# Kernel optimization log

Measured on AMD Instinct MI355X. Metric: run time of the kernel, lower is better.

## Reference

```python
import math
import jax, jax.numpy as jnp
import numpy as np

D_MODEL = 512
MAX_SEQ = 512
NUM_OUT = 16
H = 1  # num_heads


def _pos_encoding(d_model, seq_len):
    # sinusoidal PE, then flipped along the sequence axis (ReversedPositionalEncoding)
    pos = jnp.arange(seq_len, dtype=jnp.float32)[:, None]
    i = jnp.arange(0, d_model, 2, dtype=jnp.float32)
    ang = pos * jnp.exp(i * (-(math.log(10000.0) / d_model)))  # [S, d/2]
    pe = jnp.stack([jnp.sin(ang), jnp.cos(ang)], axis=-1).reshape(seq_len, d_model)
    return pe[::-1]


def _layernorm(x, w, b, eps=1e-5):
    m = jnp.mean(x, axis=-1, keepdims=True)
    v = jnp.mean(jnp.square(x - m), axis=-1, keepdims=True)
    return (x - m) / jnp.sqrt(v + eps) * w + b


def setup_inputs() -> dict:
    key = jax.random.key(0)
    ks = jax.random.split(key, 8)
    B = 128
    latents = jax.random.normal(ks[0], (B, D_MODEL, MAX_SEQ), dtype=jnp.float32)
    query_mask = jnp.ones((B, NUM_OUT), dtype=jnp.float32)
    query = 0.02 * jax.random.normal(ks[1], (NUM_OUT, D_MODEL), dtype=jnp.float32)
    return {
        "latents": latents,
        "query_mask": query_mask,
        "query": query,
        "ln_lat_w": jnp.ones((D_MODEL,), jnp.float32),
        "ln_lat_b": jnp.zeros((D_MODEL,), jnp.float32),
        "ln_q_w": jnp.ones((D_MODEL,), jnp.float32),
        "ln_q_b": jnp.zeros((D_MODEL,), jnp.float32),
        "Wq": 0.02 * jax.random.normal(ks[2], (D_MODEL, D_MODEL), jnp.float32),
        "bq": jnp.zeros((D_MODEL,), jnp.float32),
        "Wk": 0.02 * jax.random.normal(ks[3], (D_MODEL, D_MODEL), jnp.float32),
        "bk": jnp.zeros((D_MODEL,), jnp.float32),
        "Wv": 0.02 * jax.random.normal(ks[4], (D_MODEL, D_MODEL), jnp.float32),
        "bv": jnp.zeros((D_MODEL,), jnp.float32),
        "Wo": 0.02 * jax.random.normal(ks[5], (1, D_MODEL), jnp.float32),
        "bo": jnp.zeros((1,), jnp.float32),
    }


def reference(latents, query_mask, query, ln_lat_w, ln_lat_b, ln_q_w, ln_q_b,
              Wq, bq, Wk, bk, Wv, bv, Wo, bo):
    B, _, N = latents.shape  # latents: [B, d_model, N]
    scale = math.sqrt(D_MODEL)
    Dh = D_MODEL // H

    # cross-attention mask: query_mask [B,Nq] x all-ones latent mask [B,N]
    mask = jnp.einsum('bq,bk->bqk', query_mask, jnp.ones((B, N), latents.dtype))

    x = jnp.swapaxes(latents, 1, 2) * scale           # [B, N, d]
    x = x + _pos_encoding(D_MODEL, MAX_SEQ)[-N:]      # reversed PE, last N positions
    # dropout is identity in eval mode
    x = _layernorm(x, ln_lat_w, ln_lat_b)

    q = _layernorm(query * scale, ln_q_w, ln_q_b)     # [Nq, d]
    q = jnp.broadcast_to(q[None], (B, NUM_OUT, D_MODEL))

    qh = (q @ Wq.T + bq).reshape(B, NUM_OUT, H, Dh)
    kh = (x @ Wk.T + bk).reshape(B, N, H, Dh)
    vh = (x @ Wv.T + bv).reshape(B, N, H, Dh)

    scores = jnp.einsum('bqhd,bkhd->bhqk', qh, kh) / math.sqrt(Dh)
    scores = jnp.where(mask[:, None] == 0, -1e9, scores)
    attn_weights = jax.nn.softmax(scores, axis=-1)    # [B, H, Nq, N]

    attn = jnp.einsum('bhqk,bkhd->bqhd', attn_weights, vh).reshape(B, NUM_OUT, H * Dh)
    wipe = jnp.all(mask == 0, axis=2, keepdims=True)  # [B, Nq, 1]
    attn = jnp.where(wipe, 0.0, attn)

    logits = attn @ Wo.T + bo                         # [B, Nq, 1]
    return logits, attn_weights
```

## Files before the change

kernel.cpp:

```cpp
#include <hip/hip_runtime.h>
#include <math.h>

#define DM 512
#define NQ 16
#define NG (NQ + 1)
#define NR (NG + 2)

typedef __attribute__((ext_vector_type(2))) float f32x2;

__device__ __forceinline__ float wave_reduce_sum(float v) {
    #pragma unroll
    for (int off = 32; off > 0; off >>= 1) v += __shfl_xor(v, off, 64);
    return v;
}
__device__ __forceinline__ float wave_reduce_max(float v) {
    #pragma unroll
    for (int off = 32; off > 0; off >>= 1) v = fmaxf(v, __shfl_xor(v, off, 64));
    return v;
}

__global__ void k1_setup(const float* __restrict__ Wk, const float* __restrict__ Wv,
                         const float* __restrict__ query,
                         const float* __restrict__ ln_q_w, const float* __restrict__ ln_q_b,
                         const float* __restrict__ Wq, const float* __restrict__ bq,
                         float* __restrict__ PET, float* __restrict__ WkT,
                         float* __restrict__ WvT, float* __restrict__ qh, int N) {
    __shared__ float tile[64][65];
    int bx = blockIdx.x;
    int lane = threadIdx.x & 63;
    int w = threadIdx.x >> 6;

    if (bx < 128) {
        int ntile = bx & 7, jg = bx >> 3;
        int n = ntile * 64 + lane;
        float p = (float)(N - 1 - n);
        const float c = -logf(10000.f) / (float)DM;
        int jbase = jg * 16 + w * 4;
        #pragma unroll
        for (int u = 0; u < 4; ++u) {
            int j = jbase + u;
            float wj = expf((float)(2 * j) * c);
            float ang = p * wj;
            PET[(size_t)(2 * j) * N + n] = sinf(ang);
            PET[(size_t)(2 * j + 1) * N + n] = cosf(ang);
        }
    } else if (bx < 256) {
        int t = bx - 128;
        const float* W = (t >> 6) ? Wv : Wk;
        float* WT = (t >> 6) ? WvT : WkT;
        int tl = t & 63;
        int te = tl >> 3, td = tl & 7;
        #pragma unroll
        for (int i = 0; i < 16; ++i) {
            int el = w * 16 + i;
            tile[el][lane] = W[(size_t)(te * 64 + el) * DM + td * 64 + lane];
        }
        __syncthreads();
        #pragma unroll
        for (int i = 0; i < 16; ++i) {
            int dl = w * 16 + i;
            WT[(size_t)(td * 64 + dl) * DM + te * 64 + lane] = tile[lane][dl];
        }
    } else {
        int idx = (bx - 256) * 4 + w;
        int q = idx >> 9, e = idx & 511;
        const float scale = 22.627416997969522f;
        const float4* qr = (const float4*)(query + (size_t)q * DM);
        float4 a0 = qr[lane * 2], a1 = qr[lane * 2 + 1];
        a0.x *= scale; a0.y *= scale; a0.z *= scale; a0.w *= scale;
        a1.x *= scale; a1.y *= scale; a1.z *= scale; a1.w *= scale;
        float s  = a0.x + a0.y + a0.z + a0.w + a1.x + a1.y + a1.z + a1.w;
        float s2 = a0.x * a0.x + a0.y * a0.y + a0.z * a0.z + a0.w * a0.w
                 + a1.x * a1.x + a1.y * a1.y + a1.z * a1.z + a1.w * a1.w;
        s = wave_reduce_sum(s); s2 = wave_reduce_sum(s2);
        float m = s * (1.f / DM);
        float var = s2 * (1.f / DM) - m * m;
        float rstd = rsqrtf(var + 1e-5f);
        const float4* gw = (const float4*)ln_q_w;
        const float4* gb = (const float4*)ln_q_b;
        const float4* wr = (const float4*)(Wq + (size_t)e * DM);
        float4 w0 = gw[lane * 2], w1 = gw[lane * 2 + 1];
        float4 b0 = gb[lane * 2], b1 = gb[lane * 2 + 1];
        float4 W0 = wr[lane * 2], W1 = wr[lane * 2 + 1];
        float acc = ((a0.x - m) * rstd * w0.x + b0.x) * W0.x
                  + ((a0.y - m) * rstd * w0.y + b0.y) * W0.y
                  + ((a0.z - m) * rstd * w0.z + b0.z) * W0.z
                  + ((a0.w - m) * rstd * w0.w + b0.w) * W0.w
                  + ((a1.x - m) * rstd * w1.x + b1.x) * W1.x
                  + ((a1.y - m) * rstd * w1.y + b1.y) * W1.y
                  + ((a1.z - m) * rstd * w1.z + b1.z) * W1.z
                  + ((a1.w - m) * rstd * w1.w + b1.w) * W1.w;
        acc = wave_reduce_sum(acc);
        if (lane == 0) qh[q * DM + e] = acc + bq[e];
    }
}

__global__ void k3_qt(const float* __restrict__ qh, const float* __restrict__ WkT,
                      const float* __restrict__ Wo, const float* __restrict__ WvT,
                      const float* __restrict__ lnw,
                      float* __restrict__ qt, float* __restrict__ A,
                      f32x2* __restrict__ A2, float* __restrict__ wvout) {
    int idx = blockIdx.x * 4 + (threadIdx.x >> 6);
    int lane = threadIdx.x & 63;
    int g = idx >> 9, d = idx & 511;
    const float4* wr;
    const float4* xr;
    if (g < NQ) {
        wr = (const float4*)(WkT + (size_t)d * DM);
        xr = (const float4*)(qh + (size_t)g * DM);
    } else {
        wr = (const float4*)(WvT + (size_t)d * DM);
        xr = (const float4*)Wo;
    }
    float4 w0 = wr[lane * 2], w1 = wr[lane * 2 + 1];
    float4 x0 = xr[lane * 2], x1 = xr[lane * 2 + 1];
    float s = w0.x * x0.x + w0.y * x0.y + w0.z * x0.z + w0.w * x0.w
            + w1.x * x1.x + w1.y * x1.y + w1.z * x1.z + w1.w * x1.w;
    s = wave_reduce_sum(s);
    if (lane == 0) {
        if (g < NQ) qt[g * DM + d] = s;
        else wvout[d] = s;
        float a = s * lnw[d];
        A[g * DM + d] = a;
        f32x2 ap; ap.x = a; ap.y = a;
        A2[g * DM + d] = ap;
    }
}

__launch_bounds__(256, 4)
__global__ void main2_kernel(const float* __restrict__ latents,
                             const float* __restrict__ PET,
                             const f32x2* __restrict__ A2,
                             const float* __restrict__ A,
                             const float* __restrict__ qt,
                             const float* __restrict__ qh,
                             const float* __restrict__ wv,
                             const float* __restrict__ lnb,
                             const float* __restrict__ bk,
                             const float* __restrict__ Wo,
                             const float* __restrict__ bv,
                             float* __restrict__ pbuf,
                             float* __restrict__ consts, int N) {
    int B = gridDim.y - 1;
    int lane = threadIdx.x & 63;
    int w = threadIdx.x >> 6;
    int b = blockIdx.y;

    if (b == B) {
        int t = blockIdx.x * 4 + w;
        if (t > NQ) return;
        if (t < NQ) {
            float sa = 0.f, sc = 0.f, qb = 0.f;
            #pragma unroll
            for (int i = 0; i < 8; ++i) {
                int d = i * 64 + lane;
                sa += A[t * DM + d];
                sc = fmaf(qt[t * DM + d], lnb[d], sc);
                qb = fmaf(qh[t * DM + d], bk[d], qb);
            }
            sa = wave_reduce_sum(sa);
            sc = wave_reduce_sum(sc);
            qb = wave_reduce_sum(qb);
            if (lane == 0) { consts[t] = sa; consts[16 + t] = sc + qb; }
        } else {
            float sa = 0.f, cv = 0.f, bvo = 0.f;
            #pragma unroll
            for (int i = 0; i < 8; ++i) {
                int d = i * 64 + lane;
                sa += A[NQ * DM + d];
                cv = fmaf(wv[d], lnb[d], cv);
                bvo = fmaf(Wo[d], bv[d], bvo);
            }
            sa = wave_reduce_sum(sa);
            cv = wave_reduce_sum(cv);
            bvo = wave_reduce_sum(bvo);
            if (lane == 0) { consts[32] = sa; consts[33] = cv + bvo; }
        }
        return;
    }

    int ntiles = N >> 7;
    int ntile = blockIdx.x % ntiles;
    int dh = blockIdx.x / ntiles;
    int n0 = ntile * 128 + lane * 2;

    int d0 = __builtin_amdgcn_readfirstlane(dh * 256 + w * 64);
    const float* latf = latents + (size_t)b * DM * N + (size_t)d0 * N + n0;
    const float* petf = PET + (size_t)d0 * N + n0;
    const float scale = 22.627416997969522f;
    f32x2 sc2; sc2.x = scale; sc2.y = scale;

    f32x2 acc[NG];
    #pragma unroll
    for (int i = 0; i < NG; ++i) { acc[i].x = 0.f; acc[i].y = 0.f; }
    f32x2 S1 = {0.f, 0.f}, S2 = {0.f, 0.f};

    const int U = 4;
    const int NC = 64 / U;
    f32x2 xb[2][U], pb[2][U];
    #pragma unroll
    for (int u = 0; u < U; ++u) {
        xb[0][u] = __builtin_nontemporal_load((const f32x2*)(latf + (size_t)u * N));
        pb[0][u] = *(const f32x2*)(petf + (size_t)u * N);
    }
    for (int c = 0; c < NC; c += 2) {
        #pragma unroll
        for (int u = 0; u < U; ++u) {
            size_t dd = (size_t)((c + 1) * U + u) * N;
            xb[1][u] = __builtin_nontemporal_load((const f32x2*)(latf + dd));
            pb[1][u] = *(const f32x2*)(petf + dd);
        }
        #pragma unroll
        for (int u = 0; u < U; ++u) {
            f32x2 y = xb[0][u] * sc2 + pb[0][u];
            S1 += y; S2 += y * y;
            int d = d0 + c * U + u;
            #pragma unroll
            for (int q = 0; q < NG; ++q)
                acc[q] += A2[(size_t)q * DM + d] * y;
        }
        if (c + 2 < NC) {
            #pragma unroll
            for (int u = 0; u < U; ++u) {
                size_t dd = (size_t)((c + 2) * U + u) * N;
                xb[0][u] = __builtin_nontemporal_load((const f32x2*)(latf + dd));
                pb[0][u] = *(const f32x2*)(petf + dd);
            }
        }
        #pragma unroll
        for (int u = 0; u < U; ++u) {
            f32x2 y = xb[1][u] * sc2 + pb[1][u];
            S1 += y; S2 += y * y;
            int d = d0 + (c + 1) * U + u;
            #pragma unroll
            for (int q = 0; q < NG; ++q)
                acc[q] += A2[(size_t)q * DM + d] * y;
        }
    }

    __shared__ f32x2 red[4][NR][64];
    red[w][0][lane] = S1;
    red[w][1][lane] = S2;
    #pragma unroll
    for (int i = 0; i < NG; ++i) red[w][2 + i][lane] = acc[i];
    __syncthreads();
    if (w != 0) return;

    float* pout = pbuf + (((size_t)dh * B + b) * NR) * N + n0;
    #pragma unroll
    for (int i = 0; i < NR; ++i) {
        f32x2 t = red[0][i][lane] + red[1][i][lane] + red[2][i][lane] + red[3][i][lane];
        *(f32x2*)(pout + (size_t)i * N) = t;
    }
}

__global__ void k_fin(const float* __restrict__ pbuf,
                      const float* __restrict__ consts,
                      const float* __restrict__ query_mask,
                      const float* __restrict__ bo,
                      float* __restrict__ out_logits,
                      float* __restrict__ out_attn, int N, int B) {
    __shared__ float scs[NQ][512];
    __shared__ float vls[512];
    int b = blockIdx.x;
    int tid = threadIdx.x;
    const float isd = 0.044194173824159216f;
    float c32 = consts[32], c33 = consts[33];

    for (int np = tid; np < (N >> 1); np += 256) {
        int n0 = np * 2;
        const float* p0 = pbuf + (((size_t)0 * B + b) * NR) * N + n0;
        const float* p1 = pbuf + (((size_t)1 * B + b) * NR) * N + n0;
        f32x2 tot[NR];
        #pragma unroll
        for (int i = 0; i < NR; ++i)
            tot[i] = *(const f32x2*)(p0 + (size_t)i * N)
                   + *(const f32x2*)(p1 + (size_t)i * N);
        f32x2 m = tot[0] * (1.f / DM);
        f32x2 ex2 = tot[1] * (1.f / DM);
        f32x2 rstd;
        rstd.x = rsqrtf(ex2.x - m.x * m.x + 1e-5f);
        rstd.y = rsqrtf(ex2.y - m.y * m.y + 1e-5f);
        f32x2 v = rstd * (tot[2 + NQ] - m * c32) + c33;
        *(f32x2*)&vls[n0] = v;
        #pragma unroll
        for (int q = 0; q < NQ; ++q) {
            f32x2 sc = (rstd * (tot[2 + q] - m * consts[q]) + consts[16 + q]) * isd;
            *(f32x2*)&scs[q][n0] = sc;
        }
    }
    __syncthreads();

    int lane = tid & 63, w = tid >> 6;
    int nv = N >> 2;
    for (int q = w; q < NQ; q += 4) {
        int r = b * NQ + q;
        float qm = query_mask[r];
        float4* arow = (float4*)(out_attn + (size_t)r * N);
        if (qm == 0.f) {
            float u = 1.f / (float)N;
            float4 uv = make_float4(u, u, u, u);
            for (int i = lane; i < nv; i += 64) arow[i] = uv;
            if (lane == 0) out_logits[r] = bo[0];
            continue;
        }
        const float4* srow = (const float4*)scs[q];
        float4 sv[2];
        sv[0] = srow[lane]; sv[1] = srow[64 + lane];
        float mx = fmaxf(fmaxf(fmaxf(sv[0].x, sv[0].y), fmaxf(sv[0].z, sv[0].w)),
                         fmaxf(fmaxf(sv[1].x, sv[1].y), fmaxf(sv[1].z, sv[1].w)));
        mx = wave_reduce_max(mx);
        float sum = 0.f;
        #pragma unroll
        for (int i = 0; i < 2; ++i) {
            sv[i].x = expf(sv[i].x - mx); sv[i].y = expf(sv[i].y - mx);
            sv[i].z = expf(sv[i].z - mx); sv[i].w = expf(sv[i].w - mx);
            sum += sv[i].x + sv[i].y + sv[i].z + sv[i].w;
        }
        sum = wave_reduce_sum(sum);
        float inv = 1.f / sum;
        const float4* vrow = (const float4*)vls;
        float lp = 0.f;
        #pragma unroll
        for (int i = 0; i < 2; ++i) {
            float4 vv = vrow[i * 64 + lane];
            float4 wgt;
            wgt.x = sv[i].x * inv; wgt.y = sv[i].y * inv;
            wgt.z = sv[i].z * inv; wgt.w = sv[i].w * inv;
            arow[i * 64 + lane] = wgt;
            lp += wgt.x * vv.x + wgt.y * vv.y + wgt.z * vv.z + wgt.w * vv.w;
        }
        lp = wave_reduce_sum(lp);
        if (lane == 0) out_logits[r] = lp + bo[0];
    }
}

extern "C" void kernel_launch(void* const* d_in, const int* in_sizes, int n_in,
                              void* d_out, int out_size, void* d_ws, size_t ws_size,
                              hipStream_t stream) {
    const float* latents    = (const float*)d_in[0];
    const float* query_mask = (const float*)d_in[1];
    const float* query      = (const float*)d_in[2];
    const float* ln_lat_w   = (const float*)d_in[3];
    const float* ln_lat_b   = (const float*)d_in[4];
    const float* ln_q_w     = (const float*)d_in[5];
    const float* ln_q_b     = (const float*)d_in[6];
    const float* Wq         = (const float*)d_in[7];
    const float* bq         = (const float*)d_in[8];
    const float* Wk         = (const float*)d_in[9];
    const float* bk         = (const float*)d_in[10];
    const float* Wv         = (const float*)d_in[11];
    const float* bv         = (const float*)d_in[12];
    const float* Wo         = (const float*)d_in[13];
    const float* bo         = (const float*)d_in[14];

    int B = in_sizes[1] / NQ;
    int N = in_sizes[0] / (DM * B);

    float* ws = (float*)d_ws;
    size_t off = 0;
    float* PET    = ws + off; off += (size_t)DM * N;
    float* WkT    = ws + off; off += (size_t)DM * DM;
    float* WvT    = ws + off; off += (size_t)DM * DM;
    float* qh     = ws + off; off += NQ * DM;
    float* qt     = ws + off; off += NQ * DM;
    float* A      = ws + off; off += NG * DM;
    float* A2     = ws + off; off += (size_t)NG * DM * 2;
    float* wv     = ws + off; off += DM;
    float* consts = ws + off; off += 64;
    float* pbuf   = ws + off; off += (size_t)2 * B * NR * N;

    float* out_logits = (float*)d_out;
    float* out_attn   = out_logits + (size_t)B * NQ;

    k1_setup<<<256 + NQ * DM / 4, 256, 0, stream>>>(
        Wk, Wv, query, ln_q_w, ln_q_b, Wq, bq, PET, WkT, WvT, qh, N);
    k3_qt<<<NG * DM / 4, 256, 0, stream>>>(qh, WkT, Wo, WvT, ln_lat_w,
                                           qt, A, (f32x2*)A2, wv);
    dim3 gmain((N >> 7) * 2, B + 1);
    main2_kernel<<<gmain, 256, 0, stream>>>(latents, PET, (const f32x2*)A2,
                                            A, qt, qh, wv, ln_lat_b, bk, Wo, bv,
                                            pbuf, consts, N);
    k_fin<<<B, 256, 0, stream>>>(pbuf, consts, query_mask, bo,
                                 out_logits, out_attn, N, B);
}
```

Baseline: 240.9 us.

## Cover full d_model per block with 8 waves and drop split partial buffer

The main kernel now launches 512-thread blocks. Each block spans all 512 feature rows for a 128-column tile, where before two blocks each covered half the rows. The 8 wave partials are reduced in two LDS stages, so the pbuf partial buffer halves and k_fin no longer sums two halves. The attention-weight stores in k_fin become nontemporal vector stores. The main kernel gets half as many blocks, larger blocks and an extra barrier, which may lower occupancy and grid parallelism.

After: 240.0 us (median of 2 runs). No clear change (-0.4%).

```diff
diff --git a/kernel.cpp b/kernel.cpp
--- a/kernel.cpp
+++ b/kernel.cpp
@@ -7,6 +7,7 @@
 #define NR (NG + 2)
 
 typedef __attribute__((ext_vector_type(2))) float f32x2;
+typedef __attribute__((ext_vector_type(4))) float f32x4;
 
 __device__ __forceinline__ float wave_reduce_sum(float v) {
     #pragma unroll
@@ -127,7 +128,7 @@
     }
 }
 
-__launch_bounds__(256, 4)
+__launch_bounds__(512, 4)
 __global__ void main2_kernel(const float* __restrict__ latents,
                              const float* __restrict__ PET,
                              const f32x2* __restrict__ A2,
@@ -147,7 +148,7 @@
     int b = blockIdx.y;
 
     if (b == B) {
-        int t = blockIdx.x * 4 + w;
+        int t = blockIdx.x * 8 + w;
         if (t > NQ) return;
         if (t < NQ) {
             float sa = 0.f, sc = 0.f, qb = 0.f;
@@ -179,12 +180,10 @@
         return;
     }
 
-    int ntiles = N >> 7;
-    int ntile = blockIdx.x % ntiles;
-    int dh = blockIdx.x / ntiles;
+    int ntile = blockIdx.x;
     int n0 = ntile * 128 + lane * 2;
 
-    int d0 = __builtin_amdgcn_readfirstlane(dh * 256 + w * 64);
+    int d0 = __builtin_amdgcn_readfirstlane(w * 64);
     const float* latf = latents + (size_t)b * DM * N + (size_t)d0 * N + n0;
     const float* petf = PET + (size_t)d0 * N + n0;
     const float scale = 22.627416997969522f;
@@ -239,18 +238,29 @@
     }
 
     __shared__ f32x2 red[4][NR][64];
-    red[w][0][lane] = S1;
-    red[w][1][lane] = S2;
-    #pragma unroll
-    for (int i = 0; i < NG; ++i) red[w][2 + i][lane] = acc[i];
+    if (w >= 4) {
+        int ww = w - 4;
+        red[ww][0][lane] = S1;
+        red[ww][1][lane] = S2;
+        #pragma unroll
+        for (int i = 0; i < NG; ++i) red[ww][2 + i][lane] = acc[i];
+    }
     __syncthreads();
-    if (w != 0) return;
-
-    float* pout = pbuf + (((size_t)dh * B + b) * NR) * N + n0;
-    #pragma unroll
-    for (int i = 0; i < NR; ++i) {
-        f32x2 t = red[0][i][lane] + red[1][i][lane] + red[2][i][lane] + red[3][i][lane];
-        *(f32x2*)(pout + (size_t)i * N) = t;
+    if (w < 4) {
+        red[w][0][lane] += S1;
+        red[w][1][lane] += S2;
+        #pragma unroll
+        for (int i = 0; i < NG; ++i) red[w][2 + i][lane] += acc[i];
+    }
+    __syncthreads();
+    if (w == 0) {
+        float* pout = pbuf + ((size_t)b * NR) * N + n0;
+        #pragma unroll
+        for (int i = 0; i < NR; ++i) {
+            f32x2 t = red[0][i][lane] + red[1][i][lane]
+                    + red[2][i][lane] + red[3][i][lane];
+            *(f32x2*)(pout + (size_t)i * N) = t;
+        }
     }
 }
 
@@ -269,13 +279,10 @@
 
     for (int np = tid; np < (N >> 1); np += 256) {
         int n0 = np * 2;
-        const float* p0 = pbuf + (((size_t)0 * B + b) * NR) * N + n0;
-        const float* p1 = pbuf + (((size_t)1 * B + b) * NR) * N + n0;
+        const float* p = pbuf + ((size_t)b * NR) * N + n0;
         f32x2 tot[NR];
         #pragma unroll
-        for (int i = 0; i < NR; ++i)
-            tot[i] = *(const f32x2*)(p0 + (size_t)i * N)
-                   + *(const f32x2*)(p1 + (size_t)i * N);
+        for (int i = 0; i < NR; ++i) tot[i] = *(const f32x2*)(p + (size_t)i * N);
         f32x2 m = tot[0] * (1.f / DM);
         f32x2 ex2 = tot[1] * (1.f / DM);
         f32x2 rstd;
@@ -296,16 +303,17 @@
     for (int q = w; q < NQ; q += 4) {
         int r = b * NQ + q;
         float qm = query_mask[r];
-        float4* arow = (float4*)(out_attn + (size_t)r * N);
+        f32x4* arow = (f32x4*)(out_attn + (size_t)r * N);
         if (qm == 0.f) {
             float u = 1.f / (float)N;
-            float4 uv = make_float4(u, u, u, u);
-            for (int i = lane; i < nv; i += 64) arow[i] = uv;
+            f32x4 uv; uv.x = u; uv.y = u; uv.z = u; uv.w = u;
+            for (int i = lane; i < nv; i += 64)
+                __builtin_nontemporal_store(uv, &arow[i]);
             if (lane == 0) out_logits[r] = bo[0];
             continue;
         }
-        const float4* srow = (const float4*)scs[q];
-        float4 sv[2];
+        const f32x4* srow = (const f32x4*)scs[q];
+        f32x4 sv[2];
         sv[0] = srow[lane]; sv[1] = srow[64 + lane];
         float mx = fmaxf(fmaxf(fmaxf(sv[0].x, sv[0].y), fmaxf(sv[0].z, sv[0].w)),
                          fmaxf(fmaxf(sv[1].x, sv[1].y), fmaxf(sv[1].z, sv[1].w)));
@@ -319,15 +327,13 @@
         }
         sum = wave_reduce_sum(sum);
         float inv = 1.f / sum;
-        const float4* vrow = (const float4*)vls;
+        const f32x4* vrow = (const f32x4*)vls;
         float lp = 0.f;
         #pragma unroll
         for (int i = 0; i < 2; ++i) {
-            float4 vv = vrow[i * 64 + lane];
-            float4 wgt;
-            wgt.x = sv[i].x * inv; wgt.y = sv[i].y * inv;
-            wgt.z = sv[i].z * inv; wgt.w = sv[i].w * inv;
-            arow[i * 64 + lane] = wgt;
+            f32x4 vv = vrow[i * 64 + lane];
+            f32x4 wgt = sv[i] * inv;
+            __builtin_nontemporal_store(wgt, &arow[i * 64 + lane]);
             lp += wgt.x * vv.x + wgt.y * vv.y + wgt.z * vv.z + wgt.w * vv.w;
         }
         lp = wave_reduce_sum(lp);
@@ -368,7 +374,7 @@
     float* A2     = ws + off; off += (size_t)NG * DM * 2;
     float* wv     = ws + off; off += DM;
     float* consts = ws + off; off += 64;
-    float* pbuf   = ws + off; off += (size_t)2 * B * NR * N;
+    float* pbuf   = ws + off; off += (size_t)B * NR * N;
 
     float* out_logits = (float*)d_out;
     float* out_attn   = out_logits + (size_t)B * NQ;
@@ -377,8 +383,8 @@
         Wk, Wv, query, ln_q_w, ln_q_b, Wq, bq, PET, WkT, WvT, qh, N);
     k3_qt<<<NG * DM / 4, 256, 0, stream>>>(qh, WkT, Wo, WvT, ln_lat_w,
                                            qt, A, (f32x2*)A2, wv);
-    dim3 gmain((N >> 7) * 2, B + 1);
-    main2_kernel<<<gmain, 256, 0, stream>>>(latents, PET, (const f32x2*)A2,
+    dim3 gmain(N >> 7, B + 1);
+    main2_kernel<<<gmain, 512, 0, stream>>>(latents, PET, (const f32x2*)A2,
                                             A, qt, qh, wv, ln_lat_b, bk, Wo, bv,
                                             pbuf, consts, N);
     k_fin<<<B, 256, 0, stream>>>(pbuf, consts, query_mask, bo,
```
